# Kernel tuning notes

Measured on AMD Instinct MI355X. Metric: run time of the kernel, lower is better.

## Reference

```python
import jax, jax.numpy as jnp
import numpy as np

NUM_CLASS = 5000
INPUT_DIM = 1024
EMB_DIM = 512
MLP_AT_DIM = 512
CELL = 1024
OUT_DIM = 512
CLIP = 1.0
T, B, U = 500, 32, 100


def setup_inputs() -> dict:
    key = jax.random.key(0)
    ks = jax.random.split(key, 12)
    s = 0.05
    return {
        "data": jax.random.normal(ks[0], (T, B, INPUT_DIM), jnp.float32),
        "att_mask": jnp.ones((U, B), jnp.float32),
        "att_label": jax.random.randint(ks[1], (U, B), 0, NUM_CLASS - 2, jnp.int32),
        "rnn_mask": jnp.ones((T, B, 1), jnp.float32),
        "emb_W": jax.random.uniform(ks[2], (NUM_CLASS, EMB_DIM), jnp.float32, -s, s),
        "Wi2h": jax.random.uniform(ks[3], (MLP_AT_DIM, INPUT_DIM), jnp.float32, -s, s),
        "Wp2s": jax.random.uniform(ks[4], (MLP_AT_DIM, OUT_DIM), jnp.float32, -s, s),
        "w_att_v": jax.random.uniform(ks[5], (1, MLP_AT_DIM), jnp.float32, -s, s),
        "Wx": jax.random.normal(ks[6], (4 * CELL, EMB_DIM + INPUT_DIM), jnp.float32) * 0.02,
        "Wp": jax.random.normal(ks[7], (4 * CELL, OUT_DIM), jnp.float32) * 0.02,
        "b": jnp.zeros((4 * CELL,), jnp.float32),
        "Wproj": jax.random.normal(ks[8], (OUT_DIM, CELL), jnp.float32) * 0.02,
    }


def reference(data, att_mask, att_label, rnn_mask, emb_W, Wi2h, Wp2s, w_att_v, Wx, Wp, b, Wproj):
    rm = rnn_mask[: data.shape[0]].squeeze(-1)  # [T, B] (clip_mask)
    # shift labels right with sos = num_class - 2
    sos = jnp.full((1, att_label.shape[1]), NUM_CLASS - 2, att_label.dtype)
    labels = jnp.concatenate([sos, att_label[:-1]], axis=0)  # [U, B]
    # MaskEmbedding: -1 labels -> zero vector
    valid = (labels >= 0).astype(emb_W.dtype)[..., None]
    embed = emb_W[jnp.where(labels < 0, 0, labels)] * valid  # [U, B, E]
    att_h = jnp.einsum("tbi,mi->tbm", data, Wi2h)  # [T, B, M]
    mask_bias = (rm - 1.0) * 1e10  # [T, B]

    def step(carry, emb_t):
        c, p, ctx = carry
        body = jnp.concatenate([emb_t, ctx], axis=1)  # [B, E+I]
        gates = body @ Wx.T + p @ Wp.T + b  # [B, 4C]
        i_g, f_g, g_g, o_g = jnp.split(gates, 4, axis=1)
        c = jax.nn.sigmoid(f_g) * c + jax.nn.sigmoid(i_g) * jnp.tanh(g_g)
        c = jnp.clip(c, -CLIP, CLIP)
        h = jax.nn.sigmoid(o_g) * jnp.tanh(c)
        p = h @ Wproj.T  # [B, OUT]
        state = p @ Wp2s.T  # [B, M]
        out = w_att_v * jnp.tanh(state[None] + att_h)  # [T, B, M]
        scalar = jax.nn.sigmoid(out.sum(-1) + mask_bias)  # [T, B]
        ctx = (data * scalar[..., None]).sum(0)  # [B, I]
        return (c, p, ctx), (p, ctx)

    Bsz = data.shape[1]
    carry0 = (
        jnp.zeros((Bsz, CELL), data.dtype),
        jnp.zeros((Bsz, OUT_DIM), data.dtype),
        jnp.zeros((Bsz, INPUT_DIM), data.dtype),
    )
    _, (lstmps, contexts) = jax.lax.scan(step, carry0, embed)
    am = att_mask[..., None]
    return jnp.concatenate([lstmps * am, contexts * am], axis=2)  # [U, B, OUT+I]
```

## Files before the change

### kernel.cpp

```cpp
#include <hip/hip_runtime.h>
#include <hip/hip_bf16.h>

#define T_DIM 500
#define B_DIM 32
#define U_DIM 100
#define I_DIM 1024
#define E_DIM 512
#define M_DIM 512
#define CELL_DIM 1024
#define ODIM 512
#define NC 5000
#define G4 4096
#define KBODY 1536

typedef __attribute__((ext_vector_type(8))) short short8;
typedef __attribute__((ext_vector_type(4))) float f32x4;

__device__ __forceinline__ float bf2f(unsigned short u){
  union { unsigned int i; float f; } v; v.i = ((unsigned int)u) << 16; return v.f;
}
__device__ __forceinline__ unsigned short f2bf(float f){
  union { float f; unsigned int i; } v; v.f = f;
  unsigned int lsb = (v.i >> 16) & 1u;
  unsigned int r = v.i + 0x7fffu + lsb;
  return (unsigned short)(r >> 16);
}
__device__ __forceinline__ float fast_tanh(float x){
  float ax = fabsf(x);
  float e = __expf(2.0f * ax);
  float t = 1.0f - 2.0f / (e + 1.0f);
  return copysignf(t, x);
}
__device__ __forceinline__ float fast_sig(float x){
  return 1.0f / (1.0f + __expf(-x));
}


__global__ void k_cvt_bf16(const float* __restrict__ src, unsigned short* __restrict__ dst, int n4){
  int i = blockIdx.x * 256 + threadIdx.x;
  if (i >= n4) return;
  float4 v = reinterpret_cast<const float4*>(src)[i];
  ushort4 o;
  o.x = f2bf(v.x); o.y = f2bf(v.y); o.z = f2bf(v.z); o.w = f2bf(v.w);
  reinterpret_cast<ushort4*>(dst)[i] = o;
}

__global__ void k_embed(const int* __restrict__ att_label, const float* __restrict__ emb_W,
                        float* __restrict__ embed){
  int idx = blockIdx.x * 256 + threadIdx.x;
  int e  = idx & (E_DIM - 1);
  int ub = idx >> 9;
  int b  = ub & (B_DIM - 1);
  int u  = ub >> 5;
  int label = (u == 0) ? (NC - 2) : att_label[(u - 1) * B_DIM + b];
  float val = 0.0f;
  if (label >= 0) val = emb_W[label * E_DIM + e];
  embed[idx] = val;
}

__global__ void k_bias(const float* __restrict__ rnn_mask, float* __restrict__ bias){
  int idx = blockIdx.x * 256 + threadIdx.x;
  if (idx < T_DIM * B_DIM) bias[idx] = (rnn_mask[idx] - 1.0f) * 1e10f;
}

__global__ void k_wcomb(const float* __restrict__ Wp2s, const float* __restrict__ Wproj,
                        float* __restrict__ Wcomb){
  int idx = blockIdx.x * 256 + threadIdx.x;
  int c = idx & (CELL_DIM - 1);
  int m = idx >> 10;
  float acc = 0.f;
  for (int k = 0; k < ODIM; ++k)
    acc += Wp2s[m * ODIM + k] * Wproj[k * CELL_DIM + c];
  Wcomb[idx] = acc;
}

__global__ __launch_bounds__(256) void k_atth(const unsigned short* __restrict__ A,
                                              const unsigned short* __restrict__ Bm,
                                              unsigned short* __restrict__ C){
  const int mt = blockIdx.x % 250;
  const int nt = blockIdx.x / 250;
  const int wave = threadIdx.x >> 6;
  const int lane = threadIdx.x & 63;
  const int r16 = lane & 15;
  const int kl = (lane >> 4) * 8;
  const unsigned short* aptr = A + (mt * 64 + wave * 16 + r16) * 1024 + kl;
  const unsigned short* bptr = Bm + (nt * 64 + r16) * 1024 + kl;
  f32x4 acc0 = {0,0,0,0}, acc1 = {0,0,0,0}, acc2 = {0,0,0,0}, acc3 = {0,0,0,0};
  for (int kk = 0; kk < 1024; kk += 32) {
    short8 a  = *reinterpret_cast<const short8*>(aptr + kk);
    short8 b0 = *reinterpret_cast<const short8*>(bptr + kk);
    short8 b1 = *reinterpret_cast<const short8*>(bptr + 16 * 1024 + kk);
    short8 b2 = *reinterpret_cast<const short8*>(bptr + 32 * 1024 + kk);
    short8 b3 = *reinterpret_cast<const short8*>(bptr + 48 * 1024 + kk);
    acc0 = __builtin_amdgcn_mfma_f32_16x16x32_bf16(a, b0, acc0, 0, 0, 0);
    acc1 = __builtin_amdgcn_mfma_f32_16x16x32_bf16(a, b1, acc1, 0, 0, 0);
    acc2 = __builtin_amdgcn_mfma_f32_16x16x32_bf16(a, b2, acc2, 0, 0, 0);
    acc3 = __builtin_amdgcn_mfma_f32_16x16x32_bf16(a, b3, acc3, 0, 0, 0);
  }
  const int orow = mt * 64 + wave * 16 + (lane >> 4) * 4;
  const int ocol = nt * 64 + r16;
  #pragma unroll
  for (int r = 0; r < 4; ++r) {
    C[(orow + r) * 512 + ocol]      = f2bf(acc0[r]);
    C[(orow + r) * 512 + ocol + 16] = f2bf(acc1[r]);
    C[(orow + r) * 512 + ocol + 32] = f2bf(acc2[r]);
    C[(orow + r) * 512 + ocol + 48] = f2bf(acc3[r]);
  }
}


__global__ __launch_bounds__(256) void k_gates(const float* __restrict__ embed_u,
    const float* __restrict__ ctx, const float* __restrict__ pprev,
    const float* __restrict__ Wx, const float* __restrict__ Wp,
    const float* __restrict__ bvec, float* __restrict__ gates){
  __shared__ float s_x[32][140];
  const int tid = threadIdx.x;
  const int n = blockIdx.x * 8 + (tid & 7);
  const int b = tid >> 3;
  float acc = bvec[n];
  for (int ch = 0; ch < 12; ++ch) {
    #pragma unroll
    for (int i = 0; i < 4; ++i) {
      int fidx = tid + i * 256;
      int bb = fidx >> 5;
      int kk4 = (fidx & 31) * 4;
      int k = ch * 128 + kk4;
      float4 v;
      if (k < 512) v = *reinterpret_cast<const float4*>(embed_u + bb * E_DIM + k);
      else         v = *reinterpret_cast<const float4*>(ctx + bb * I_DIM + (k - 512));
      *reinterpret_cast<float4*>(&s_x[bb][kk4]) = v;
    }
    __syncthreads();
    const float* wrow = Wx + n * KBODY + ch * 128;
    for (int kk = 0; kk < 128; kk += 4) {
      float4 xv = *reinterpret_cast<const float4*>(&s_x[b][kk]);
      float4 wv = *reinterpret_cast<const float4*>(wrow + kk);
      acc += xv.x * wv.x + xv.y * wv.y + xv.z * wv.z + xv.w * wv.w;
    }
    __syncthreads();
  }
  for (int ch = 0; ch < 4; ++ch) {
    #pragma unroll
    for (int i = 0; i < 4; ++i) {
      int fidx = tid + i * 256;
      int bb = fidx >> 5;
      int kk4 = (fidx & 31) * 4;
      int k = ch * 128 + kk4;
      float4 v = *reinterpret_cast<const float4*>(pprev + bb * ODIM + k);
      *reinterpret_cast<float4*>(&s_x[bb][kk4]) = v;
    }
    __syncthreads();
    const float* wrow = Wp + n * ODIM + ch * 128;
    for (int kk = 0; kk < 128; kk += 4) {
      float4 xv = *reinterpret_cast<const float4*>(&s_x[b][kk]);
      float4 wv = *reinterpret_cast<const float4*>(wrow + kk);
      acc += xv.x * wv.x + xv.y * wv.y + xv.z * wv.z + xv.w * wv.w;
    }
    __syncthreads();
  }
  gates[b * G4 + n] = acc;
}

__global__ void k_cell(const float* __restrict__ gates, float* __restrict__ c_ws,
                       float* __restrict__ h_ws){
  int idx = blockIdx.x * 256 + threadIdx.x;
  int b = idx >> 10;
  int j = idx & 1023;
  const float* g = gates + b * G4;
  float ig = fast_sig(g[j]);
  float fg = fast_sig(g[1024 + j]);
  float gg = fast_tanh(g[2048 + j]);
  float og = fast_sig(g[3072 + j]);
  float c = fg * c_ws[idx] + ig * gg;
  c = fminf(fmaxf(c, -1.0f), 1.0f);
  c_ws[idx] = c;
  h_ws[idx] = og * fast_tanh(c);
}

__global__ __launch_bounds__(256) void k_ps(const float* __restrict__ h_ws,
    const float* __restrict__ Wproj, const float* __restrict__ Wcomb,
    float* __restrict__ p_ws, float* __restrict__ state_ws,
    float* __restrict__ out, const float* __restrict__ att_mask, int u){
  __shared__ float s_h[32][140];
  const int tid = threadIdx.x;
  const int n = blockIdx.x * 8 + (tid & 7);
  const int b = tid >> 3;
  float acc = 0.f;
  const float* wrow = (n < 512) ? (Wproj + n * CELL_DIM) : (Wcomb + (n - 512) * CELL_DIM);
  for (int ch = 0; ch < 8; ++ch) {
    #pragma unroll
    for (int i = 0; i < 4; ++i) {
      int fidx = tid + i * 256;
      int bb = fidx >> 5;
      int kk4 = (fidx & 31) * 4;
      float4 v = *reinterpret_cast<const float4*>(h_ws + bb * CELL_DIM + ch * 128 + kk4);
      *reinterpret_cast<float4*>(&s_h[bb][kk4]) = v;
    }
    __syncthreads();
    const float* w = wrow + ch * 128;
    for (int kk = 0; kk < 128; kk += 4) {
      float4 xv = *reinterpret_cast<const float4*>(&s_h[b][kk]);
      float4 wv = *reinterpret_cast<const float4*>(w + kk);
      acc += xv.x * wv.x + xv.y * wv.y + xv.z * wv.z + xv.w * wv.w;
    }
    __syncthreads();
  }
  if (n < 512) {
    p_ws[b * ODIM + n] = acc;
    out[(u * B_DIM + b) * 1536 + n] = acc * att_mask[u * B_DIM + b];
  } else {
    state_ws[b * M_DIM + (n - 512)] = acc;
  }
}

__global__ __launch_bounds__(256) void k_scalar(const unsigned short* __restrict__ att_h,
    const float* __restrict__ state_ws, const float* __restrict__ w_v,
    const float* __restrict__ bias, float* __restrict__ scal){
  const int lane = threadIdx.x & 63;
  const int tb = blockIdx.x * 4 + (threadIdx.x >> 6);
  const int b = tb & 31;
  const int m0 = lane * 8;
  const unsigned short* ap = att_h + tb * 512 + m0;
  ushort4 a0 = *reinterpret_cast<const ushort4*>(ap);
  ushort4 a1 = *reinterpret_cast<const ushort4*>(ap + 4);
  float4 s0 = *reinterpret_cast<const float4*>(state_ws + b * 512 + m0);
  float4 s1 = *reinterpret_cast<const float4*>(state_ws + b * 512 + m0 + 4);
  float4 w0 = *reinterpret_cast<const float4*>(w_v + m0);
  float4 w1 = *reinterpret_cast<const float4*>(w_v + m0 + 4);
  float acc = w0.x * fast_tanh(s0.x + bf2f(a0.x))
            + w0.y * fast_tanh(s0.y + bf2f(a0.y))
            + w0.z * fast_tanh(s0.z + bf2f(a0.z))
            + w0.w * fast_tanh(s0.w + bf2f(a0.w))
            + w1.x * fast_tanh(s1.x + bf2f(a1.x))
            + w1.y * fast_tanh(s1.y + bf2f(a1.y))
            + w1.z * fast_tanh(s1.z + bf2f(a1.z))
            + w1.w * fast_tanh(s1.w + bf2f(a1.w));
  #pragma unroll
  for (int off = 32; off >= 1; off >>= 1)
    acc += __shfl_xor(acc, off, 64);
  if (lane == 0)
    scal[tb] = fast_sig(acc + bias[tb]);
}

__global__ __launch_bounds__(256) void k_ctx_part(const unsigned short* __restrict__ data_bf,
    const float* __restrict__ scal, float* __restrict__ part){
  __shared__ float s_s[128];
  const int tc = blockIdx.x >> 5;
  const int b = blockIdx.x & 31;
  const int tid = threadIdx.x;
  if (tid < 125) s_s[tid] = scal[(tc * 125 + tid) * B_DIM + b];
  __syncthreads();
  const int i0 = tid * 4;
  float4 acc = {0, 0, 0, 0};
  const unsigned short* dp = data_bf + ((size_t)(tc * 125 * B_DIM + b)) * I_DIM + i0;
  #pragma unroll 5
  for (int tt = 0; tt < 125; ++tt) {
    ushort4 v = *reinterpret_cast<const ushort4*>(dp);
    float s = s_s[tt];
    acc.x += bf2f(v.x) * s;
    acc.y += bf2f(v.y) * s;
    acc.z += bf2f(v.z) * s;
    acc.w += bf2f(v.w) * s;
    dp += B_DIM * I_DIM;
  }
  *reinterpret_cast<float4*>(part + (tc * B_DIM + b) * I_DIM + i0) = acc;
}

__global__ void k_ctx_final(const float* __restrict__ part, float* __restrict__ ctx,
    float* __restrict__ out, const float* __restrict__ att_mask, int u){
  int idx = blockIdx.x * 256 + threadIdx.x;
  int b = idx >> 10;
  int i = idx & 1023;
  float v = part[idx] + part[32 * 1024 + idx] + part[2 * 32 * 1024 + idx] + part[3 * 32 * 1024 + idx];
  ctx[idx] = v;
  out[(u * B_DIM + b) * 1536 + 512 + i] = v * att_mask[u * B_DIM + b];
}

extern "C" void kernel_launch(void* const* d_in, const int* in_sizes, int n_in,
                              void* d_out, int out_size, void* d_ws, size_t ws_size,
                              hipStream_t stream) {
  const float* data     = (const float*)d_in[0];
  const float* att_mask = (const float*)d_in[1];
  const int*   att_label= (const int*)d_in[2];
  const float* rnn_mask = (const float*)d_in[3];
  const float* emb_W    = (const float*)d_in[4];
  const float* Wi2h     = (const float*)d_in[5];
  const float* Wp2s     = (const float*)d_in[6];
  const float* w_att_v  = (const float*)d_in[7];
  const float* Wx       = (const float*)d_in[8];
  const float* Wp       = (const float*)d_in[9];
  const float* bvec     = (const float*)d_in[10];
  const float* Wproj    = (const float*)d_in[11];
  float* out = (float*)d_out;

  char* ws = (char*)d_ws;
  size_t off = 0;
  auto alloc = [&](size_t bytes){ void* p = ws + off; off += (bytes + 255) & ~(size_t)255; return p; };
  unsigned short* data_bf = (unsigned short*)alloc((size_t)T_DIM * B_DIM * I_DIM * 2);
  unsigned short* atth_bf = (unsigned short*)alloc((size_t)T_DIM * B_DIM * M_DIM * 2);
  unsigned short* Wi2h_bf = (unsigned short*)alloc((size_t)M_DIM * I_DIM * 2);
  float* embed    = (float*)alloc((size_t)U_DIM * B_DIM * E_DIM * 4);
  float* bias     = (float*)alloc((size_t)T_DIM * B_DIM * 4);
  float* Wcomb    = (float*)alloc((size_t)M_DIM * CELL_DIM * 4);
  float* c_ws     = (float*)alloc((size_t)B_DIM * CELL_DIM * 4);
  float* h_ws     = (float*)alloc((size_t)B_DIM * CELL_DIM * 4);
  float* p_ws     = (float*)alloc((size_t)B_DIM * ODIM * 4);
  float* ctx_ws   = (float*)alloc((size_t)B_DIM * I_DIM * 4);
  float* state_ws = (float*)alloc((size_t)B_DIM * M_DIM * 4);
  float* gates    = (float*)alloc((size_t)B_DIM * G4 * 4);
  float* scal     = (float*)alloc((size_t)T_DIM * B_DIM * 4);
  float* part     = (float*)alloc((size_t)4 * B_DIM * I_DIM * 4);

  hipMemsetAsync(c_ws, 0, (size_t)B_DIM * CELL_DIM * 4, stream);
  hipMemsetAsync(p_ws, 0, (size_t)B_DIM * ODIM * 4, stream);
  hipMemsetAsync(ctx_ws, 0, (size_t)B_DIM * I_DIM * 4, stream);

  k_cvt_bf16<<<(T_DIM * B_DIM * I_DIM / 4 + 255) / 256, 256, 0, stream>>>(data, data_bf, T_DIM * B_DIM * I_DIM / 4);
  k_cvt_bf16<<<(M_DIM * I_DIM / 4 + 255) / 256, 256, 0, stream>>>(Wi2h, Wi2h_bf, M_DIM * I_DIM / 4);
  k_atth<<<2000, 256, 0, stream>>>(data_bf, Wi2h_bf, atth_bf);
  k_embed<<<U_DIM * B_DIM * E_DIM / 256, 256, 0, stream>>>(att_label, emb_W, embed);
  k_bias<<<(T_DIM * B_DIM + 255) / 256, 256, 0, stream>>>(rnn_mask, bias);
  k_wcomb<<<M_DIM * CELL_DIM / 256, 256, 0, stream>>>(Wp2s, Wproj, Wcomb);

  for (int u = 0; u < U_DIM; ++u) {
    k_gates<<<512, 256, 0, stream>>>(embed + (size_t)u * B_DIM * E_DIM, ctx_ws, p_ws, Wx, Wp, bvec, gates);
    k_cell<<<128, 256, 0, stream>>>(gates, c_ws, h_ws);
    k_ps<<<128, 256, 0, stream>>>(h_ws, Wproj, Wcomb, p_ws, state_ws, out, att_mask, u);
    k_scalar<<<4000, 256, 0, stream>>>(atth_bf, state_ws, w_att_v, bias, scal);
    k_ctx_part<<<128, 256, 0, stream>>>(data_bf, scal, part);
    k_ctx_final<<<128, 256, 0, stream>>>(part, ctx_ws, out, att_mask, u);
  }
}
```

Baseline: 20.41 ms.

## Fuse recurrent loop into one persistent cooperative kernel with bf16 MFMA GEMMs

Replaces the 600 per-step kernel launches with a single cooperative kernel of 512 blocks. It loops over all 100 decoder steps and uses grid.sync between phases: gates plus LSTM cell, projection and state, attention scalars, then context. The gate and projection matmuls now use bf16 MFMA on weights packed once up front. Context partial sums go through atomicAdd into a zeroed ctx buffer. This removes launch overhead and intermediate gates/h round trips, at the cost of bf16 precision for the recurrent weights and activations and grid-wide barriers that leave many blocks idle in some phases.

```diff
diff --git a/kernel.cpp b/kernel.cpp
--- a/kernel.cpp
+++ b/kernel.cpp
@@ -1,5 +1,8 @@
 #include <hip/hip_runtime.h>
 #include <hip/hip_bf16.h>
+#include <hip/hip_cooperative_groups.h>
+
+namespace cg = cooperative_groups;
 
 #define T_DIM 500
 #define B_DIM 32
@@ -11,7 +14,7 @@
 #define ODIM 512
 #define NC 5000
 #define G4 4096
-#define KBODY 1536
+#define KBODY 2048
 
 typedef __attribute__((ext_vector_type(8))) short short8;
 typedef __attribute__((ext_vector_type(4))) float f32x4;
@@ -33,6 +36,14 @@
 }
 __device__ __forceinline__ float fast_sig(float x){
   return 1.0f / (1.0f + __expf(-x));
+}
+__device__ __forceinline__ short8 cvt8_bf(const float* p){
+  float4 c0 = *reinterpret_cast<const float4*>(p);
+  float4 c1 = *reinterpret_cast<const float4*>(p + 4);
+  short8 a;
+  a[0]=(short)f2bf(c0.x); a[1]=(short)f2bf(c0.y); a[2]=(short)f2bf(c0.z); a[3]=(short)f2bf(c0.w);
+  a[4]=(short)f2bf(c1.x); a[5]=(short)f2bf(c1.y); a[6]=(short)f2bf(c1.z); a[7]=(short)f2bf(c1.w);
+  return a;
 }
 
 
@@ -45,8 +56,8 @@
   reinterpret_cast<ushort4*>(dst)[i] = o;
 }
 
-__global__ void k_embed(const int* __restrict__ att_label, const float* __restrict__ emb_W,
-                        float* __restrict__ embed){
+__global__ void k_embed_bf(const int* __restrict__ att_label, const float* __restrict__ emb_W,
+                           unsigned short* __restrict__ embed_bf){
   int idx = blockIdx.x * 256 + threadIdx.x;
   int e  = idx & (E_DIM - 1);
   int ub = idx >> 9;
@@ -55,7 +66,7 @@
   int label = (u == 0) ? (NC - 2) : att_label[(u - 1) * B_DIM + b];
   float val = 0.0f;
   if (label >= 0) val = emb_W[label * E_DIM + e];
-  embed[idx] = val;
+  embed_bf[idx] = f2bf(val);
 }
 
 __global__ void k_bias(const float* __restrict__ rnn_mask, float* __restrict__ bias){
@@ -72,6 +83,28 @@
   for (int k = 0; k < ODIM; ++k)
     acc += Wp2s[m * ODIM + k] * Wproj[k * CELL_DIM + c];
   Wcomb[idx] = acc;
+}
+
+__global__ void k_pack_wg(const float* __restrict__ Wx, const float* __restrict__ Wp,
+                          unsigned short* __restrict__ Wg){
+  int idx4 = blockIdx.x * 256 + threadIdx.x;
+  int n = idx4 >> 9;
+  int k = (idx4 & 511) * 4;
+  float4 v = (k < 1536) ? *reinterpret_cast<const float4*>(Wx + n * 1536 + k)
+                        : *reinterpret_cast<const float4*>(Wp + n * 512 + (k - 1536));
+  ushort4 o; o.x = f2bf(v.x); o.y = f2bf(v.y); o.z = f2bf(v.z); o.w = f2bf(v.w);
+  *reinterpret_cast<ushort4*>(Wg + n * 2048 + k) = o;
+}
+
+__global__ void k_pack_wpc(const float* __restrict__ Wproj, const float* __restrict__ Wcomb,
+                           unsigned short* __restrict__ Wpc){
+  int idx4 = blockIdx.x * 256 + threadIdx.x;
+  int n = idx4 >> 8;
+  int k = (idx4 & 255) * 4;
+  const float* src = (n < 512) ? (Wproj + n * 1024 + k) : (Wcomb + (n - 512) * 1024 + k);
+  float4 v = *reinterpret_cast<const float4*>(src);
+  ushort4 o; o.x = f2bf(v.x); o.y = f2bf(v.y); o.z = f2bf(v.z); o.w = f2bf(v.w);
+  *reinterpret_cast<ushort4*>(Wpc + n * 1024 + k) = o;
 }
 
 __global__ __launch_bounds__(256) void k_atth(const unsigned short* __restrict__ A,
@@ -108,172 +141,196 @@
   }
 }
 
-
-__global__ __launch_bounds__(256) void k_gates(const float* __restrict__ embed_u,
-    const float* __restrict__ ctx, const float* __restrict__ pprev,
-    const float* __restrict__ Wx, const float* __restrict__ Wp,
-    const float* __restrict__ bvec, float* __restrict__ gates){
-  __shared__ float s_x[32][140];
+__global__ __launch_bounds__(256, 2) void k_loop(
+    const unsigned short* __restrict__ data_bf,
+    const unsigned short* __restrict__ atth_bf,
+    const unsigned short* __restrict__ embed_bf,
+    const float* __restrict__ bias,
+    const unsigned short* __restrict__ Wg,
+    const unsigned short* __restrict__ Wpc,
+    const float* __restrict__ bvec,
+    const float* __restrict__ w_v,
+    const float* __restrict__ att_mask,
+    float* __restrict__ c_ws,
+    unsigned short* __restrict__ h_bf,
+    unsigned short* __restrict__ p_bf,
+    float* __restrict__ state,
+    float* __restrict__ ctx,
+    float* __restrict__ scal,
+    float* __restrict__ out)
+{
+  cg::grid_group grid = cg::this_grid();
+  const int bid = blockIdx.x;
   const int tid = threadIdx.x;
-  const int n = blockIdx.x * 8 + (tid & 7);
-  const int b = tid >> 3;
-  float acc = bvec[n];
-  for (int ch = 0; ch < 12; ++ch) {
-    #pragma unroll
-    for (int i = 0; i < 4; ++i) {
-      int fidx = tid + i * 256;
-      int bb = fidx >> 5;
-      int kk4 = (fidx & 31) * 4;
-      int k = ch * 128 + kk4;
-      float4 v;
-      if (k < 512) v = *reinterpret_cast<const float4*>(embed_u + bb * E_DIM + k);
-      else         v = *reinterpret_cast<const float4*>(ctx + bb * I_DIM + (k - 512));
-      *reinterpret_cast<float4*>(&s_x[bb][kk4]) = v;
+  const int wv = tid >> 6;
+  const int lane = tid & 63;
+  const int r16 = lane & 15;
+  const int khi = lane >> 4;
+
+  __shared__ float s_g[4][16][16];
+  __shared__ float s_s[64];
+
+  for (int u = 0; u < U_DIM; ++u) {
+    if (bid < 128) {
+      const int mt = bid >> 6;
+      const int jt = bid & 63;
+      const unsigned short* brow = Wg + ((size_t)(wv * 1024 + jt * 16 + r16)) * KBODY + khi * 8;
+      const int arow = mt * 16 + r16;
+      const unsigned short* aemb = embed_bf + ((size_t)(u * 32 + arow)) * 512 + khi * 8;
+      const float* actx = ctx + arow * 1024 + khi * 8;
+      const unsigned short* ap = p_bf + arow * 512 + khi * 8;
+      f32x4 acc0 = {0,0,0,0}, acc1 = {0,0,0,0};
+      #pragma unroll 4
+      for (int ks = 0; ks < 16; ks += 2) {
+        short8 a0 = *reinterpret_cast<const short8*>(aemb + ks * 32);
+        short8 b0 = *reinterpret_cast<const short8*>(brow + ks * 32);
+        short8 a1 = *reinterpret_cast<const short8*>(aemb + ks * 32 + 32);
+        short8 b1 = *reinterpret_cast<const short8*>(brow + ks * 32 + 32);
+        acc0 = __builtin_amdgcn_mfma_f32_16x16x32_bf16(a0, b0, acc0, 0, 0, 0);
+        acc1 = __builtin_amdgcn_mfma_f32_16x16x32_bf16(a1, b1, acc1, 0, 0, 0);
+      }
+      #pragma unroll 4
+      for (int ks = 0; ks < 32; ks += 2) {
+        short8 a0 = cvt8_bf(actx + ks * 32);
+        short8 b0 = *reinterpret_cast<const short8*>(brow + 512 + ks * 32);
+        short8 a1 = cvt8_bf(actx + ks * 32 + 32);
+        short8 b1 = *reinterpret_cast<const short8*>(brow + 512 + ks * 32 + 32);
+        acc0 = __builtin_amdgcn_mfma_f32_16x16x32_bf16(a0, b0, acc0, 0, 0, 0);
+        acc1 = __builtin_amdgcn_mfma_f32_16x16x32_bf16(a1, b1, acc1, 0, 0, 0);
+      }
+      #pragma unroll 4
+      for (int ks = 0; ks < 16; ks += 2) {
+        short8 a0 = *reinterpret_cast<const short8*>(ap + ks * 32);
+        short8 b0 = *reinterpret_cast<const short8*>(brow + 1536 + ks * 32);
+        short8 a1 = *reinterpret_cast<const short8*>(ap + ks * 32 + 32);
+        short8 b1 = *reinterpret_cast<const short8*>(brow + 1536 + ks * 32 + 32);
+        acc0 = __builtin_amdgcn_mfma_f32_16x16x32_bf16(a0, b0, acc0, 0, 0, 0);
+        acc1 = __builtin_amdgcn_mfma_f32_16x16x32_bf16(a1, b1, acc1, 0, 0, 0);
+      }
+      const float bv = bvec[wv * 1024 + jt * 16 + r16];
+      #pragma unroll
+      for (int r = 0; r < 4; ++r)
+        s_g[wv][khi * 4 + r][r16] = acc0[r] + acc1[r] + bv;
+      __syncthreads();
+      const int b_loc = tid >> 4, j_loc = tid & 15;
+      float ig = fast_sig(s_g[0][b_loc][j_loc]);
+      float fg = fast_sig(s_g[1][b_loc][j_loc]);
+      float gg = fast_tanh(s_g[2][b_loc][j_loc]);
+      float og = fast_sig(s_g[3][b_loc][j_loc]);
+      const int idx = (mt * 16 + b_loc) * 1024 + jt * 16 + j_loc;
+      float c = fg * c_ws[idx] + ig * gg;
+      c = fminf(fmaxf(c, -1.0f), 1.0f);
+      c_ws[idx] = c;
+      h_bf[idx] = f2bf(og * fast_tanh(c));
+      __syncthreads();
+    } else if (bid >= 128 && bid < 160) {
+      if (u > 0) {
+        const int b = bid - 128;
+        const float am = att_mask[(u - 1) * 32 + b];
+        float4 v = *reinterpret_cast<const float4*>(ctx + b * 1024 + tid * 4);
+        float4 o; o.x = v.x * am; o.y = v.y * am; o.z = v.z * am; o.w = v.w * am;
+        *reinterpret_cast<float4*>(out + ((size_t)(u - 1) * 32 + b) * 1536 + 512 + tid * 4) = o;
+      }
     }
-    __syncthreads();
-    const float* wrow = Wx + n * KBODY + ch * 128;
-    for (int kk = 0; kk < 128; kk += 4) {
-      float4 xv = *reinterpret_cast<const float4*>(&s_x[b][kk]);
-      float4 wv = *reinterpret_cast<const float4*>(wrow + kk);
-      acc += xv.x * wv.x + xv.y * wv.y + xv.z * wv.z + xv.w * wv.w;
+    grid.sync();
+
+    if (bid < 32) {
+      const int task = bid * 4 + wv;
+      const int mt = task & 1, nt = task >> 1;
+      const unsigned short* brow = Wpc + ((size_t)(nt * 16 + r16)) * 1024 + khi * 8;
+      const unsigned short* arow = h_bf + ((size_t)(mt * 16 + r16)) * 1024 + khi * 8;
+      f32x4 acc0 = {0,0,0,0}, acc1 = {0,0,0,0};
+      #pragma unroll 4
+      for (int ks = 0; ks < 32; ks += 2) {
+        short8 a0 = *reinterpret_cast<const short8*>(arow + ks * 32);
+        short8 b0 = *reinterpret_cast<const short8*>(brow + ks * 32);
+        short8 a1 = *reinterpret_cast<const short8*>(arow + ks * 32 + 32);
+        short8 b1 = *reinterpret_cast<const short8*>(brow + ks * 32 + 32);
+        acc0 = __builtin_amdgcn_mfma_f32_16x16x32_bf16(a0, b0, acc0, 0, 0, 0);
+        acc1 = __builtin_amdgcn_mfma_f32_16x16x32_bf16(a1, b1, acc1, 0, 0, 0);
+      }
+      const int n = nt * 16 + r16;
+      #pragma unroll
+      for (int r = 0; r < 4; ++r) {
+        const int b = mt * 16 + khi * 4 + r;
+        const float v = acc0[r] + acc1[r];
+        if (n < 512) {
+          p_bf[b * 512 + n] = f2bf(v);
+          out[((size_t)u * 32 + b) * 1536 + n] = v * att_mask[u * 32 + b];
+        } else {
+          state[b * 512 + (n - 512)] = v;
+        }
+      }
+    } else if (bid >= 480) {
+      float4 z = {0.f, 0.f, 0.f, 0.f};
+      *reinterpret_cast<float4*>(ctx + (bid - 480) * 1024 + tid * 4) = z;
     }
-    __syncthreads();
+    grid.sync();
+
+    {
+      const int wg = bid * 4 + wv;
+      const int m0 = lane * 8;
+      for (int r = wg; r < T_DIM * B_DIM; r += 2048) {
+        const int b = r & 31;
+        const unsigned short* apt = atth_bf + (size_t)r * 512 + m0;
+        ushort4 a0 = *reinterpret_cast<const ushort4*>(apt);
+        ushort4 a1 = *reinterpret_cast<const ushort4*>(apt + 4);
+        float4 s0 = *reinterpret_cast<const float4*>(state + b * 512 + m0);
+        float4 s1 = *reinterpret_cast<const float4*>(state + b * 512 + m0 + 4);
+        float4 w0 = *reinterpret_cast<const float4*>(w_v + m0);
+        float4 w1 = *reinterpret_cast<const float4*>(w_v + m0 + 4);
+        float acc = w0.x * fast_tanh(s0.x + bf2f(a0.x))
+                  + w0.y * fast_tanh(s0.y + bf2f(a0.y))
+                  + w0.z * fast_tanh(s0.z + bf2f(a0.z))
+                  + w0.w * fast_tanh(s0.w + bf2f(a0.w))
+                  + w1.x * fast_tanh(s1.x + bf2f(a1.x))
+                  + w1.y * fast_tanh(s1.y + bf2f(a1.y))
+                  + w1.z * fast_tanh(s1.z + bf2f(a1.z))
+                  + w1.w * fast_tanh(s1.w + bf2f(a1.w));
+        #pragma unroll
+        for (int off = 32; off >= 1; off >>= 1)
+          acc += __shfl_xor(acc, off, 64);
+        if (lane == 0)
+          scal[r] = fast_sig(acc + bias[r]);
+      }
+    }
+    grid.sync();
+
+    if (bid < 320) {
+      const int tc = bid >> 5;
+      const int b  = bid & 31;
+      if (tid < 50) s_s[tid] = scal[(tc * 50 + tid) * 32 + b];
+      __syncthreads();
+      const int i0 = tid * 4;
+      float4 acc = {0.f, 0.f, 0.f, 0.f};
+      const unsigned short* dp = data_bf + ((size_t)(tc * 50 * 32 + b)) * 1024 + i0;
+      #pragma unroll 5
+      for (int tt = 0; tt < 50; ++tt) {
+        ushort4 v = *reinterpret_cast<const ushort4*>(dp);
+        const float s = s_s[tt];
+        acc.x += bf2f(v.x) * s;
+        acc.y += bf2f(v.y) * s;
+        acc.z += bf2f(v.z) * s;
+        acc.w += bf2f(v.w) * s;
+        dp += 32 * 1024;
+      }
+      float* cp = ctx + b * 1024 + i0;
+      atomicAdd(cp + 0, acc.x);
+      atomicAdd(cp + 1, acc.y);
+      atomicAdd(cp + 2, acc.z);
+      atomicAdd(cp + 3, acc.w);
+      __syncthreads();
+    }
+    grid.sync();
   }
-  for (int ch = 0; ch < 4; ++ch) {
-    #pragma unroll
-    for (int i = 0; i < 4; ++i) {
-      int fidx = tid + i * 256;
-      int bb = fidx >> 5;
-      int kk4 = (fidx & 31) * 4;
-      int k = ch * 128 + kk4;
-      float4 v = *reinterpret_cast<const float4*>(pprev + bb * ODIM + k);
-      *reinterpret_cast<float4*>(&s_x[bb][kk4]) = v;
-    }
-    __syncthreads();
-    const float* wrow = Wp + n * ODIM + ch * 128;
-    for (int kk = 0; kk < 128; kk += 4) {
-      float4 xv = *reinterpret_cast<const float4*>(&s_x[b][kk]);
-      float4 wv = *reinterpret_cast<const float4*>(wrow + kk);
-      acc += xv.x * wv.x + xv.y * wv.y + xv.z * wv.z + xv.w * wv.w;
-    }
-    __syncthreads();
+
+  if (bid >= 128 && bid < 160) {
+    const int b = bid - 128;
+    const float am = att_mask[99 * 32 + b];
+    float4 v = *reinterpret_cast<const float4*>(ctx + b * 1024 + tid * 4);
+    float4 o; o.x = v.x * am; o.y = v.y * am; o.z = v.z * am; o.w = v.w * am;
+    *reinterpret_cast<float4*>(out + ((size_t)99 * 32 + b) * 1536 + 512 + tid * 4) = o;
   }
-  gates[b * G4 + n] = acc;
-}
-
-__global__ void k_cell(const float* __restrict__ gates, float* __restrict__ c_ws,
-                       float* __restrict__ h_ws){
-  int idx = blockIdx.x * 256 + threadIdx.x;
-  int b = idx >> 10;
-  int j = idx & 1023;
-  const float* g = gates + b * G4;
-  float ig = fast_sig(g[j]);
-  float fg = fast_sig(g[1024 + j]);
-  float gg = fast_tanh(g[2048 + j]);
-  float og = fast_sig(g[3072 + j]);
-  float c = fg * c_ws[idx] + ig * gg;
-  c = fminf(fmaxf(c, -1.0f), 1.0f);
-  c_ws[idx] = c;
-  h_ws[idx] = og * fast_tanh(c);
-}
-
-__global__ __launch_bounds__(256) void k_ps(const float* __restrict__ h_ws,
-    const float* __restrict__ Wproj, const float* __restrict__ Wcomb,
-    float* __restrict__ p_ws, float* __restrict__ state_ws,
-    float* __restrict__ out, const float* __restrict__ att_mask, int u){
-  __shared__ float s_h[32][140];
-  const int tid = threadIdx.x;
-  const int n = blockIdx.x * 8 + (tid & 7);
-  const int b = tid >> 3;
-  float acc = 0.f;
-  const float* wrow = (n < 512) ? (Wproj + n * CELL_DIM) : (Wcomb + (n - 512) * CELL_DIM);
-  for (int ch = 0; ch < 8; ++ch) {
-    #pragma unroll
-    for (int i = 0; i < 4; ++i) {
-      int fidx = tid + i * 256;
-      int bb = fidx >> 5;
-      int kk4 = (fidx & 31) * 4;
-      float4 v = *reinterpret_cast<const float4*>(h_ws + bb * CELL_DIM + ch * 128 + kk4);
-      *reinterpret_cast<float4*>(&s_h[bb][kk4]) = v;
-    }
-    __syncthreads();
-    const float* w = wrow + ch * 128;
-    for (int kk = 0; kk < 128; kk += 4) {
-      float4 xv = *reinterpret_cast<const float4*>(&s_h[b][kk]);
-      float4 wv = *reinterpret_cast<const float4*>(w + kk);
-      acc += xv.x * wv.x + xv.y * wv.y + xv.z * wv.z + xv.w * wv.w;
-    }
-    __syncthreads();
-  }
-  if (n < 512) {
-    p_ws[b * ODIM + n] = acc;
-    out[(u * B_DIM + b) * 1536 + n] = acc * att_mask[u * B_DIM + b];
-  } else {
-    state_ws[b * M_DIM + (n - 512)] = acc;
-  }
-}
-
-__global__ __launch_bounds__(256) void k_scalar(const unsigned short* __restrict__ att_h,
-    const float* __restrict__ state_ws, const float* __restrict__ w_v,
-    const float* __restrict__ bias, float* __restrict__ scal){
-  const int lane = threadIdx.x & 63;
-  const int tb = blockIdx.x * 4 + (threadIdx.x >> 6);
-  const int b = tb & 31;
-  const int m0 = lane * 8;
-  const unsigned short* ap = att_h + tb * 512 + m0;
-  ushort4 a0 = *reinterpret_cast<const ushort4*>(ap);
-  ushort4 a1 = *reinterpret_cast<const ushort4*>(ap + 4);
-  float4 s0 = *reinterpret_cast<const float4*>(state_ws + b * 512 + m0);
-  float4 s1 = *reinterpret_cast<const float4*>(state_ws + b * 512 + m0 + 4);
-  float4 w0 = *reinterpret_cast<const float4*>(w_v + m0);
-  float4 w1 = *reinterpret_cast<const float4*>(w_v + m0 + 4);
-  float acc = w0.x * fast_tanh(s0.x + bf2f(a0.x))
-            + w0.y * fast_tanh(s0.y + bf2f(a0.y))
-            + w0.z * fast_tanh(s0.z + bf2f(a0.z))
-            + w0.w * fast_tanh(s0.w + bf2f(a0.w))
-            + w1.x * fast_tanh(s1.x + bf2f(a1.x))
-            + w1.y * fast_tanh(s1.y + bf2f(a1.y))
-            + w1.z * fast_tanh(s1.z + bf2f(a1.z))
-            + w1.w * fast_tanh(s1.w + bf2f(a1.w));
-  #pragma unroll
-  for (int off = 32; off >= 1; off >>= 1)
-    acc += __shfl_xor(acc, off, 64);
-  if (lane == 0)
-    scal[tb] = fast_sig(acc + bias[tb]);
-}
-
-__global__ __launch_bounds__(256) void k_ctx_part(const unsigned short* __restrict__ data_bf,
-    const float* __restrict__ scal, float* __restrict__ part){
-  __shared__ float s_s[128];
-  const int tc = blockIdx.x >> 5;
-  const int b = blockIdx.x & 31;
-  const int tid = threadIdx.x;
-  if (tid < 125) s_s[tid] = scal[(tc * 125 + tid) * B_DIM + b];
-  __syncthreads();
-  const int i0 = tid * 4;
-  float4 acc = {0, 0, 0, 0};
-  const unsigned short* dp = data_bf + ((size_t)(tc * 125 * B_DIM + b)) * I_DIM + i0;
-  #pragma unroll 5
-  for (int tt = 0; tt < 125; ++tt) {
-    ushort4 v = *reinterpret_cast<const ushort4*>(dp);
-    float s = s_s[tt];
-    acc.x += bf2f(v.x) * s;
-    acc.y += bf2f(v.y) * s;
-    acc.z += bf2f(v.z) * s;
-    acc.w += bf2f(v.w) * s;
-    dp += B_DIM * I_DIM;
-  }
-  *reinterpret_cast<float4*>(part + (tc * B_DIM + b) * I_DIM + i0) = acc;
-}
-
-__global__ void k_ctx_final(const float* __restrict__ part, float* __restrict__ ctx,
-    float* __restrict__ out, const float* __restrict__ att_mask, int u){
-  int idx = blockIdx.x * 256 + threadIdx.x;
-  int b = idx >> 10;
-  int i = idx & 1023;
-  float v = part[idx] + part[32 * 1024 + idx] + part[2 * 32 * 1024 + idx] + part[3 * 32 * 1024 + idx];
-  ctx[idx] = v;
-  out[(u * B_DIM + b) * 1536 + 512 + i] = v * att_mask[u * B_DIM + b];
 }
 
 extern "C" void kernel_launch(void* const* d_in, const int* in_sizes, int n_in,
@@ -299,35 +356,36 @@
   unsigned short* data_bf = (unsigned short*)alloc((size_t)T_DIM * B_DIM * I_DIM * 2);
   unsigned short* atth_bf = (unsigned short*)alloc((size_t)T_DIM * B_DIM * M_DIM * 2);
   unsigned short* Wi2h_bf = (unsigned short*)alloc((size_t)M_DIM * I_DIM * 2);
-  float* embed    = (float*)alloc((size_t)U_DIM * B_DIM * E_DIM * 4);
+  unsigned short* embed_bf= (unsigned short*)alloc((size_t)U_DIM * B_DIM * E_DIM * 2);
+  unsigned short* Wg_bf   = (unsigned short*)alloc((size_t)G4 * KBODY * 2);
+  unsigned short* Wpc_bf  = (unsigned short*)alloc((size_t)1024 * 1024 * 2);
   float* bias     = (float*)alloc((size_t)T_DIM * B_DIM * 4);
   float* Wcomb    = (float*)alloc((size_t)M_DIM * CELL_DIM * 4);
   float* c_ws     = (float*)alloc((size_t)B_DIM * CELL_DIM * 4);
-  float* h_ws     = (float*)alloc((size_t)B_DIM * CELL_DIM * 4);
-  float* p_ws     = (float*)alloc((size_t)B_DIM * ODIM * 4);
+  float* state_ws = (float*)alloc((size_t)B_DIM * M_DIM * 4);
   float* ctx_ws   = (float*)alloc((size_t)B_DIM * I_DIM * 4);
-  float* state_ws = (float*)alloc((size_t)B_DIM * M_DIM * 4);
-  float* gates    = (float*)alloc((size_t)B_DIM * G4 * 4);
   float* scal     = (float*)alloc((size_t)T_DIM * B_DIM * 4);
-  float* part     = (float*)alloc((size_t)4 * B_DIM * I_DIM * 4);
+  unsigned short* h_bf = (unsigned short*)alloc((size_t)B_DIM * CELL_DIM * 2);
+  unsigned short* p_bf = (unsigned short*)alloc((size_t)B_DIM * ODIM * 2);
 
   hipMemsetAsync(c_ws, 0, (size_t)B_DIM * CELL_DIM * 4, stream);
-  hipMemsetAsync(p_ws, 0, (size_t)B_DIM * ODIM * 4, stream);
   hipMemsetAsync(ctx_ws, 0, (size_t)B_DIM * I_DIM * 4, stream);
+  hipMemsetAsync(p_bf, 0, (size_t)B_DIM * ODIM * 2, stream);
 
   k_cvt_bf16<<<(T_DIM * B_DIM * I_DIM / 4 + 255) / 256, 256, 0, stream>>>(data, data_bf, T_DIM * B_DIM * I_DIM / 4);
   k_cvt_bf16<<<(M_DIM * I_DIM / 4 + 255) / 256, 256, 0, stream>>>(Wi2h, Wi2h_bf, M_DIM * I_DIM / 4);
   k_atth<<<2000, 256, 0, stream>>>(data_bf, Wi2h_bf, atth_bf);
-  k_embed<<<U_DIM * B_DIM * E_DIM / 256, 256, 0, stream>>>(att_label, emb_W, embed);
+  k_embed_bf<<<U_DIM * B_DIM * E_DIM / 256, 256, 0, stream>>>(att_label, emb_W, embed_bf);
   k_bias<<<(T_DIM * B_DIM + 255) / 256, 256, 0, stream>>>(rnn_mask, bias);
   k_wcomb<<<M_DIM * CELL_DIM / 256, 256, 0, stream>>>(Wp2s, Wproj, Wcomb);
-
-  for (int u = 0; u < U_DIM; ++u) {
-    k_gates<<<512, 256, 0, stream>>>(embed + (size_t)u * B_DIM * E_DIM, ctx_ws, p_ws, Wx, Wp, bvec, gates);
-    k_cell<<<128, 256, 0, stream>>>(gates, c_ws, h_ws);
-    k_ps<<<128, 256, 0, stream>>>(h_ws, Wproj, Wcomb, p_ws, state_ws, out, att_mask, u);
-    k_scalar<<<4000, 256, 0, stream>>>(atth_bf, state_ws, w_att_v, bias, scal);
-    k_ctx_part<<<128, 256, 0, stream>>>(data_bf, scal, part);
-    k_ctx_final<<<128, 256, 0, stream>>>(part, ctx_ws, out, att_mask, u);
-  }
-}
+  k_pack_wg<<<G4 * (KBODY / 4) / 256, 256, 0, stream>>>(Wx, Wp, Wg_bf);
+  k_pack_wpc<<<1024 * 256 / 256, 256, 0, stream>>>(Wproj, Wcomb, Wpc_bf);
+
+  void* args[] = {
+    (void*)&data_bf, (void*)&atth_bf, (void*)&embed_bf, (void*)&bias,
+    (void*)&Wg_bf, (void*)&Wpc_bf, (void*)&bvec, (void*)&w_att_v, (void*)&att_mask,
+    (void*)&c_ws, (void*)&h_bf, (void*)&p_bf, (void*)&state_ws, (void*)&ctx_ws,
+    (void*)&scal, (void*)&out
+  };
+  hipLaunchCooperativeKernel((const void*)k_loop, dim3(512), dim3(256), args, 0, stream);
+}
```

After: 26.94 ms. +32.0%, slower.
